# Kernel tuning notes

Hardware: AMD Instinct MI355X
Metric: run time of the kernel (lower is better)

Reference implementation:

```python
import jax, jax.numpy as jnp
import numpy as np

B, S, D, H = 1, 4096, 1024, 16
HD = D // H  # head_dim = 64


def setup_inputs() -> dict:
    key = jax.random.key(0)
    k1, k2, k3 = jax.random.split(key, 3)
    scale = 0.02
    return {
        "x": jax.random.normal(k1, (B, S, D), dtype=jnp.float32),
        "w_qkv": jax.random.normal(k2, (D, 3 * D), dtype=jnp.float32) * scale,
        "b_qkv": jnp.zeros((3 * D,), dtype=jnp.float32),
        "w_proj": jax.random.normal(k3, (D, D), dtype=jnp.float32) * scale,
        "b_proj": jnp.zeros((D,), dtype=jnp.float32),
    }


def reference(x, w_qkv, b_qkv, w_proj, b_proj):
    b, s, d = x.shape
    qkv = x @ w_qkv + b_qkv                      # [b, s, 3d]
    q, k, v = jnp.split(qkv, 3, axis=-1)
    # [b, h, s, hd]
    q = q.reshape(b, s, H, HD).transpose(0, 2, 1, 3)
    k = k.reshape(b, s, H, HD).transpose(0, 2, 1, 3)
    v = v.reshape(b, s, H, HD).transpose(0, 2, 1, 3)
    score = jnp.einsum("bhqd,bhkd->bhqk", q, k) / jnp.sqrt(jnp.float32(HD))
    causal = jnp.tril(jnp.ones((s, s), dtype=bool))
    score = jnp.where(causal, score, -jnp.inf)
    attn = jax.nn.softmax(score, axis=-1)        # dropout omitted (eval mode, p effectively 0)
    out = jnp.einsum("bhqk,bhkd->bhqd", attn, v)  # [b, h, s, hd]
    out = out.transpose(0, 2, 1, 3).reshape(b, s, d)
    return out @ w_proj + b_proj
```

## Files before the change

kernel.cpp:

```cpp
#include <hip/hip_runtime.h>
#include <hip/hip_bf16.h>
#include <math.h>

typedef __bf16 bf16;
typedef __bf16 bf16x8 __attribute__((ext_vector_type(8)));
typedef __bf16 bf16x4 __attribute__((ext_vector_type(4)));
typedef float f32x4 __attribute__((ext_vector_type(4)));

#define S_ 4096
#define D_ 1024
#define H_ 16
#define HD_ 64
#define N3_ 3072

typedef const __attribute__((address_space(1))) void* gas1_t;
typedef __attribute__((address_space(3))) void* las3_t;
static __device__ __forceinline__ void g2l16(const void* g, void* l) {
  __builtin_amdgcn_global_load_lds((gas1_t)g, (las3_t)l, 16, 0, 0);
}

__global__ __launch_bounds__(256) void cvt_f32_bf16(const float* __restrict__ in,
                                                    bf16* __restrict__ out) {
  int i = (blockIdx.x * 256 + threadIdx.x) * 4;
  float4 v = *(const float4*)(in + i);
  bf16x4 o;
  o.x = (bf16)v.x; o.y = (bf16)v.y; o.z = (bf16)v.z; o.w = (bf16)v.w;
  *(bf16x4*)(out + i) = o;
}

__global__ __launch_bounds__(256) void transpose_f32_bf16(const float* __restrict__ in,
                                                          bf16* __restrict__ out,
                                                          int R, int C, int ldin, int col0) {
  __shared__ float t[32][33];
  int bx = blockIdx.x * 32;
  int by = blockIdx.y * 32;
  int tx = threadIdx.x & 31, ty = threadIdx.x >> 5;
#pragma unroll
  for (int i = 0; i < 4; ++i)
    t[ty + i * 8][tx] = in[(size_t)(by + ty + i * 8) * ldin + col0 + bx + tx];
  __syncthreads();
#pragma unroll
  for (int i = 0; i < 4; ++i)
    out[(size_t)(bx + ty + i * 8) * R + by + tx] = (bf16)t[tx][ty + i * 8];
}

__global__ __launch_bounds__(256) void transpose_bf16(const bf16* __restrict__ in,
                                                      bf16* __restrict__ out,
                                                      int R, int C, int ldin, int col0) {
  __shared__ bf16 t[32][33];
  int bx = blockIdx.x * 32;
  int by = blockIdx.y * 32;
  int tx = threadIdx.x & 31, ty = threadIdx.x >> 5;
#pragma unroll
  for (int i = 0; i < 4; ++i)
    t[ty + i * 8][tx] = in[(size_t)(by + ty + i * 8) * ldin + col0 + bx + tx];
  __syncthreads();
#pragma unroll
  for (int i = 0; i < 4; ++i)
    out[(size_t)(bx + ty + i * 8) * R + by + tx] = t[tx][ty + i * 8];
}

__global__ __launch_bounds__(256) void gemm_bt(const bf16* __restrict__ A,
                                               const bf16* __restrict__ Bt,
                                               const float* __restrict__ bias,
                                               bf16* __restrict__ outb,
                                               float* __restrict__ outf,
                                               int M, int N, int K) {
  __shared__ bf16 sA[128 * 32];
  __shared__ bf16 sB[128 * 32];
  const int tid = threadIdx.x;
  const int wave = tid >> 6, lane = tid & 63;
  const int col = lane & 15, quad = lane >> 4;
  const int wm = (wave & 1) * 64, wn = (wave >> 1) * 64;
  const long bm = (long)blockIdx.x * 128, bn = (long)blockIdx.y * 128;
  const int srow = tid >> 2;
  const int soff = (tid & 3) * 8;

  f32x4 acc[4][4] = {};

  for (int kb = 0; kb < K; kb += 32) {
    __syncthreads();
    g2l16(A  + (bm + srow) * (long)K + kb + soff,      &sA[tid * 8]);
    g2l16(A  + (bm + 64 + srow) * (long)K + kb + soff, &sA[2048 + tid * 8]);
    g2l16(Bt + (bn + srow) * (long)K + kb + soff,      &sB[tid * 8]);
    g2l16(Bt + (bn + 64 + srow) * (long)K + kb + soff, &sB[2048 + tid * 8]);
    __syncthreads();

    bf16x8 af[4], bfr[4];
#pragma unroll
    for (int t = 0; t < 4; ++t) {
      af[t]  = *(const bf16x8*)(&sA[(wm + t * 16 + col) * 32 + quad * 8]);
      bfr[t] = *(const bf16x8*)(&sB[(wn + t * 16 + col) * 32 + quad * 8]);
    }
#pragma unroll
    for (int mt = 0; mt < 4; ++mt)
#pragma unroll
      for (int nt = 0; nt < 4; ++nt)
        acc[mt][nt] = __builtin_amdgcn_mfma_f32_16x16x32_bf16(af[mt], bfr[nt], acc[mt][nt], 0, 0, 0);
  }

#pragma unroll
  for (int mt = 0; mt < 4; ++mt) {
#pragma unroll
    for (int nt = 0; nt < 4; ++nt) {
      long gn = bn + wn + nt * 16 + col;
      float bv = bias ? bias[gn] : 0.f;
#pragma unroll
      for (int i = 0; i < 4; ++i) {
        long gm = bm + wm + mt * 16 + quad * 4 + i;
        float v = acc[mt][nt][i] + bv;
        if (outf) outf[gm * N + gn] = v;
        else      outb[gm * N + gn] = (bf16)v;
      }
    }
  }
}

__device__ __forceinline__ int swz_g(int row) {
  return (row & 3) | ((((row >> 2) ^ (row >> 3)) & 1) << 2);
}

__global__ __launch_bounds__(256) void attn_kernel(const bf16* __restrict__ qkv,
                                                   const bf16* __restrict__ vT,
                                                   bf16* __restrict__ Opart,
                                                   float* __restrict__ lws) {
  __shared__ bf16 sK[2][64 * 64];
  __shared__ bf16 sV[2][64 * 64];
  const int hh = blockIdx.x;
  const int qb = (int)(gridDim.y - 1 - blockIdx.y);
  const int sp = blockIdx.z;
  const int tid = threadIdx.x;
  const int wave = tid >> 6, lane = tid & 63;
  const int col = lane & 15, quad = lane >> 4;
  const int qbase = qb * 128 + wave * 32;

  const bf16* qp0 = qkv + (size_t)(qbase + col) * N3_ + hh * HD_;
  bf16x8 aq[2][2];
  aq[0][0] = *(const bf16x8*)(qp0 + quad * 8);
  aq[0][1] = *(const bf16x8*)(qp0 + 32 + quad * 8);
  aq[1][0] = *(const bf16x8*)(qp0 + 16 * N3_ + quad * 8);
  aq[1][1] = *(const bf16x8*)(qp0 + 16 * N3_ + 32 + quad * 8);

  f32x4 acc[2][4] = {};
  float l_part[2] = {0.f, 0.f};

  const bf16* kgbase = qkv + D_ + hh * HD_;
  const bf16* vgbase = vT + (size_t)hh * HD_ * S_;
  const int krow = (col >> 2) * 8 + (col & 3);
  const float CSCALE = 0.125f * 1.44269504088896f;
  const int it0 = sp ? (qb + 1) : 0;
  const int it1 = sp ? 2 * (qb + 1) : (qb + 1);

  const int srow = tid >> 2;
  const int sc0 = (tid & 3) * 2;
  const int gs = swz_g(srow);
  const int soff0 = srow * 64 + ((sc0 ^ gs) * 8);
  const int soff1 = srow * 64 + (((sc0 + 1) ^ gs) * 8);

  {
    const bf16* kg = kgbase + (size_t)(it0 * 64 + srow) * N3_ + sc0 * 8;
    const bf16* vg = vgbase + (size_t)srow * S_ + it0 * 64 + sc0 * 8;
    *(int4*)(&sK[0][soff0]) = *(const int4*)kg;
    *(int4*)(&sK[0][soff1]) = *(const int4*)(kg + 8);
    *(int4*)(&sV[0][soff0]) = *(const int4*)vg;
    *(int4*)(&sV[0][soff1]) = *(const int4*)(vg + 8);
  }
  __syncthreads();

  for (int j = it0; j < it1; ++j) {
    const int kb = j * 64;
    const int cur = (j - it0) & 1;
    const bool more = (j + 1 < it1);
    int4 pk0, pk1, pv0, pv1;
    if (more) {
      const bf16* kg = kgbase + (size_t)(kb + 64 + srow) * N3_ + sc0 * 8;
      const bf16* vg = vgbase + (size_t)srow * S_ + kb + 64 + sc0 * 8;
      pk0 = *(const int4*)kg; pk1 = *(const int4*)(kg + 8);
      pv0 = *(const int4*)vg; pv1 = *(const int4*)(vg + 8);
    }

    if (kb < qbase + 32) {
      const bool act0 = kb < qbase + 16;
      const bf16* kc = &sK[cur][0];
      const bf16* vc = &sV[cur][0];

      f32x4 st[2][4];
#pragma unroll
      for (int t = 0; t < 4; ++t) {
        int row = (t >> 1) * 32 + (t & 1) * 4 + krow;
        int pc = quad ^ swz_g(row);
        bf16x8 bk0 = *(const bf16x8*)(kc + row * 64 + pc * 8);
        bf16x8 bk1 = *(const bf16x8*)(kc + row * 64 + (pc ^ 4) * 8);
        if (act0) {
          f32x4 z = {};
          z = __builtin_amdgcn_mfma_f32_16x16x32_bf16(bk0, aq[0][0], z, 0, 0, 0);
          st[0][t] = __builtin_amdgcn_mfma_f32_16x16x32_bf16(bk1, aq[0][1], z, 0, 0, 0);
        }
        f32x4 z = {};
        z = __builtin_amdgcn_mfma_f32_16x16x32_bf16(bk0, aq[1][0], z, 0, 0, 0);
        st[1][t] = __builtin_amdgcn_mfma_f32_16x16x32_bf16(bk1, aq[1][1], z, 0, 0, 0);
      }

      bf16x8 pfrag[2][2];
#pragma unroll
      for (int s2 = 0; s2 < 2; ++s2) {
        if (s2 == 0 && !act0) continue;
        const int rowbase = qbase + 16 * s2;
        float p[4][4];
        if (kb + 63 <= rowbase) {
#pragma unroll
          for (int t = 0; t < 4; ++t)
#pragma unroll
            for (int r = 0; r < 4; ++r)
              p[t][r] = __builtin_amdgcn_exp2f(st[s2][t][r] * CSCALE);
        } else {
#pragma unroll
          for (int t = 0; t < 4; ++t)
#pragma unroll
            for (int r = 0; r < 4; ++r) {
              int key = kb + (t >> 1) * 32 + quad * 8 + (t & 1) * 4 + r;
              p[t][r] = (key > rowbase + col)
                            ? 0.f
                            : __builtin_amdgcn_exp2f(st[s2][t][r] * CSCALE);
            }
        }
#pragma unroll
        for (int t = 0; t < 4; ++t)
#pragma unroll
          for (int r = 0; r < 4; ++r) l_part[s2] += p[t][r];
#pragma unroll
        for (int c = 0; c < 2; ++c)
#pragma unroll
          for (int j2 = 0; j2 < 4; ++j2) {
            pfrag[s2][c][j2]     = (bf16)p[2 * c][j2];
            pfrag[s2][c][j2 + 4] = (bf16)p[2 * c + 1][j2];
          }
      }

#pragma unroll
      for (int c = 0; c < 2; ++c) {
#pragma unroll
        for (int n = 0; n < 4; ++n) {
          int row = n * 16 + col;
          int pc = (4 * c + quad) ^ swz_g(row);
          bf16x8 bv = *(const bf16x8*)(vc + row * 64 + pc * 8);
          if (act0)
            acc[0][n] = __builtin_amdgcn_mfma_f32_16x16x32_bf16(pfrag[0][c], bv, acc[0][n], 0, 0, 0);
          acc[1][n] = __builtin_amdgcn_mfma_f32_16x16x32_bf16(pfrag[1][c], bv, acc[1][n], 0, 0, 0);
        }
      }
    }

    if (more) {
      bf16* kn = &sK[cur ^ 1][0];
      bf16* vn = &sV[cur ^ 1][0];
      *(int4*)(kn + soff0) = pk0;
      *(int4*)(kn + soff1) = pk1;
      *(int4*)(vn + soff0) = pv0;
      *(int4*)(vn + soff1) = pv1;
    }
    __syncthreads();
  }

  bf16* Op = Opart + (size_t)sp * S_ * D_;
#pragma unroll
  for (int s2 = 0; s2 < 2; ++s2) {
    float l = l_part[s2];
    l += __shfl_xor(l, 16);
    l += __shfl_xor(l, 32);
    if (quad == 0)
      lws[((size_t)sp * H_ + hh) * S_ + qbase + 16 * s2 + col] = l;
#pragma unroll
    for (int n = 0; n < 4; ++n)
#pragma unroll
      for (int r = 0; r < 4; ++r)
        Op[(size_t)(qbase + 16 * s2 + quad * 4 + r) * D_ + hh * HD_ + n * 16 + col] =
            (bf16)acc[s2][n][r];
  }
}

__global__ __launch_bounds__(256) void attn_combine(const bf16* __restrict__ Opart,
                                                    const float* __restrict__ lws,
                                                    bf16* __restrict__ outb) {
  int e = (blockIdx.x * 256 + threadIdx.x) * 8;
  int s = e >> 10;
  int d = e & (D_ - 1);
  int h = d >> 6;
  float l = lws[(size_t)h * S_ + s] + lws[((size_t)H_ + h) * S_ + s];
  float inv = 1.0f / l;
  bf16x8 a = *(const bf16x8*)(Opart + e);
  bf16x8 b = *(const bf16x8*)(Opart + (size_t)S_ * D_ + e);
  bf16x8 o;
#pragma unroll
  for (int j = 0; j < 8; ++j)
    o[j] = (bf16)(((float)a[j] + (float)b[j]) * inv);
  *(bf16x8*)(outb + e) = o;
}

extern "C" void kernel_launch(void* const* d_in, const int* in_sizes, int n_in,
                              void* d_out, int out_size, void* d_ws, size_t ws_size,
                              hipStream_t stream) {
  const float* x      = (const float*)d_in[0];
  const float* w_qkv  = (const float*)d_in[1];
  const float* b_qkv  = (const float*)d_in[2];
  const float* w_proj = (const float*)d_in[3];
  const float* b_proj = (const float*)d_in[4];
  float* out = (float*)d_out;

  bf16* xb     = (bf16*)d_ws;
  bf16* wqkvT  = xb + (size_t)S_ * D_;
  bf16* wprojT = wqkvT + (size_t)N3_ * D_;
  bf16* qkv    = wprojT + (size_t)D_ * D_;
  bf16* vT     = qkv + (size_t)S_ * N3_;
  bf16* attn   = vT + (size_t)D_ * S_;
  bf16* Opart  = attn + (size_t)S_ * D_;
  float* lws   = (float*)(Opart + (size_t)2 * S_ * D_);

  cvt_f32_bf16<<<dim3((S_ * D_) / 1024), 256, 0, stream>>>(x, xb);
  transpose_f32_bf16<<<dim3(N3_ / 32, D_ / 32), 256, 0, stream>>>(w_qkv, wqkvT, D_, N3_, N3_, 0);
  transpose_f32_bf16<<<dim3(D_ / 32, D_ / 32), 256, 0, stream>>>(w_proj, wprojT, D_, D_, D_, 0);
  gemm_bt<<<dim3(S_ / 128, N3_ / 128), 256, 0, stream>>>(xb, wqkvT, b_qkv, qkv, nullptr,
                                                         S_, N3_, D_);
  transpose_bf16<<<dim3(D_ / 32, S_ / 32), 256, 0, stream>>>(qkv, vT, S_, D_, N3_, 2 * D_);
  attn_kernel<<<dim3(H_, S_ / 128, 2), 256, 0, stream>>>(qkv, vT, Opart, lws);
  attn_combine<<<dim3((S_ * D_) / 2048), 256, 0, stream>>>(Opart, lws, attn);
  gemm_bt<<<dim3(S_ / 128, D_ / 128), 256, 0, stream>>>(attn, wprojT, b_proj, nullptr, out,
                                                        S_, D_, D_);
}
```

Measured before the change: 223.2 us.

## Fold softmax scale into QKV GEMM, compute row sums via MFMA, narrow proj tile

The softmax scale (1/sqrt(hd)·log2e) is now applied to Q in the QKV GEMM epilogue, so the attention inner loop no longer multiplies every score before exp2. Per-row sums of P are computed with an extra MFMA against a ones vector instead of scalar adds plus cross-lane shuffles. The GEMM is templated on the N tile, and the output projection uses a 64-wide tile to launch more blocks. The trade-offs are extra MFMA work in the attention loop and Q being rounded to bf16 after scaling, which changes rounding slightly.

```diff
diff --git a/kernel.cpp b/kernel.cpp
--- a/kernel.cpp
+++ b/kernel.cpp
@@ -60,55 +60,61 @@
     out[(size_t)(bx + ty + i * 8) * R + by + tx] = t[tx][ty + i * 8];
 }
 
+template <int BN>
 __global__ __launch_bounds__(256) void gemm_bt(const bf16* __restrict__ A,
                                                const bf16* __restrict__ Bt,
                                                const float* __restrict__ bias,
                                                bf16* __restrict__ outb,
                                                float* __restrict__ outf,
-                                               int M, int N, int K) {
+                                               int M, int N, int K,
+                                               int qlim, float qscale) {
+  constexpr int NT = BN / 32;
   __shared__ bf16 sA[128 * 32];
-  __shared__ bf16 sB[128 * 32];
+  __shared__ bf16 sB[BN * 32];
   const int tid = threadIdx.x;
   const int wave = tid >> 6, lane = tid & 63;
   const int col = lane & 15, quad = lane >> 4;
-  const int wm = (wave & 1) * 64, wn = (wave >> 1) * 64;
-  const long bm = (long)blockIdx.x * 128, bn = (long)blockIdx.y * 128;
+  const int wm = (wave & 1) * 64, wn = (wave >> 1) * (BN / 2);
+  const long bm = (long)blockIdx.x * 128, bn = (long)blockIdx.y * BN;
   const int srow = tid >> 2;
   const int soff = (tid & 3) * 8;
 
-  f32x4 acc[4][4] = {};
+  f32x4 acc[4][NT] = {};
 
   for (int kb = 0; kb < K; kb += 32) {
     __syncthreads();
-    g2l16(A  + (bm + srow) * (long)K + kb + soff,      &sA[tid * 8]);
-    g2l16(A  + (bm + 64 + srow) * (long)K + kb + soff, &sA[2048 + tid * 8]);
-    g2l16(Bt + (bn + srow) * (long)K + kb + soff,      &sB[tid * 8]);
-    g2l16(Bt + (bn + 64 + srow) * (long)K + kb + soff, &sB[2048 + tid * 8]);
+    g2l16(A + (bm + srow) * (long)K + kb + soff,      &sA[tid * 8]);
+    g2l16(A + (bm + 64 + srow) * (long)K + kb + soff, &sA[2048 + tid * 8]);
+#pragma unroll
+    for (int i = 0; i < BN / 64; ++i)
+      g2l16(Bt + (bn + i * 64 + srow) * (long)K + kb + soff, &sB[i * 2048 + tid * 8]);
     __syncthreads();
 
-    bf16x8 af[4], bfr[4];
-#pragma unroll
-    for (int t = 0; t < 4; ++t) {
-      af[t]  = *(const bf16x8*)(&sA[(wm + t * 16 + col) * 32 + quad * 8]);
+    bf16x8 af[4], bfr[NT];
+#pragma unroll
+    for (int t = 0; t < 4; ++t)
+      af[t] = *(const bf16x8*)(&sA[(wm + t * 16 + col) * 32 + quad * 8]);
+#pragma unroll
+    for (int t = 0; t < NT; ++t)
       bfr[t] = *(const bf16x8*)(&sB[(wn + t * 16 + col) * 32 + quad * 8]);
-    }
 #pragma unroll
     for (int mt = 0; mt < 4; ++mt)
 #pragma unroll
-      for (int nt = 0; nt < 4; ++nt)
+      for (int nt = 0; nt < NT; ++nt)
         acc[mt][nt] = __builtin_amdgcn_mfma_f32_16x16x32_bf16(af[mt], bfr[nt], acc[mt][nt], 0, 0, 0);
   }
 
 #pragma unroll
   for (int mt = 0; mt < 4; ++mt) {
 #pragma unroll
-    for (int nt = 0; nt < 4; ++nt) {
+    for (int nt = 0; nt < NT; ++nt) {
       long gn = bn + wn + nt * 16 + col;
       float bv = bias ? bias[gn] : 0.f;
+      float sc = (gn < qlim) ? qscale : 1.0f;
 #pragma unroll
       for (int i = 0; i < 4; ++i) {
         long gm = bm + wm + mt * 16 + quad * 4 + i;
-        float v = acc[mt][nt][i] + bv;
+        float v = (acc[mt][nt][i] + bv) * sc;
         if (outf) outf[gm * N + gn] = v;
         else      outb[gm * N + gn] = (bf16)v;
       }
@@ -141,13 +147,16 @@
   aq[1][0] = *(const bf16x8*)(qp0 + 16 * N3_ + quad * 8);
   aq[1][1] = *(const bf16x8*)(qp0 + 16 * N3_ + 32 + quad * 8);
 
+  bf16x8 ones;
+#pragma unroll
+  for (int j = 0; j < 8; ++j) ones[j] = (bf16)1.0f;
+
   f32x4 acc[2][4] = {};
-  float l_part[2] = {0.f, 0.f};
+  f32x4 acc_l[2] = {};
 
   const bf16* kgbase = qkv + D_ + hh * HD_;
   const bf16* vgbase = vT + (size_t)hh * HD_ * S_;
   const int krow = (col >> 2) * 8 + (col & 3);
-  const float CSCALE = 0.125f * 1.44269504088896f;
   const int it0 = sp ? (qb + 1) : 0;
   const int it1 = sp ? 2 * (qb + 1) : (qb + 1);
 
@@ -212,7 +221,7 @@
           for (int t = 0; t < 4; ++t)
 #pragma unroll
             for (int r = 0; r < 4; ++r)
-              p[t][r] = __builtin_amdgcn_exp2f(st[s2][t][r] * CSCALE);
+              p[t][r] = __builtin_amdgcn_exp2f(st[s2][t][r]);
         } else {
 #pragma unroll
           for (int t = 0; t < 4; ++t)
@@ -221,13 +230,9 @@
               int key = kb + (t >> 1) * 32 + quad * 8 + (t & 1) * 4 + r;
               p[t][r] = (key > rowbase + col)
                             ? 0.f
-                            : __builtin_amdgcn_exp2f(st[s2][t][r] * CSCALE);
+                            : __builtin_amdgcn_exp2f(st[s2][t][r]);
             }
         }
-#pragma unroll
-        for (int t = 0; t < 4; ++t)
-#pragma unroll
-          for (int r = 0; r < 4; ++r) l_part[s2] += p[t][r];
 #pragma unroll
         for (int c = 0; c < 2; ++c)
 #pragma unroll
@@ -248,6 +253,9 @@
             acc[0][n] = __builtin_amdgcn_mfma_f32_16x16x32_bf16(pfrag[0][c], bv, acc[0][n], 0, 0, 0);
           acc[1][n] = __builtin_amdgcn_mfma_f32_16x16x32_bf16(pfrag[1][c], bv, acc[1][n], 0, 0, 0);
         }
+        if (act0)
+          acc_l[0] = __builtin_amdgcn_mfma_f32_16x16x32_bf16(pfrag[0][c], ones, acc_l[0], 0, 0, 0);
+        acc_l[1] = __builtin_amdgcn_mfma_f32_16x16x32_bf16(pfrag[1][c], ones, acc_l[1], 0, 0, 0);
       }
     }
 
@@ -265,16 +273,17 @@
   bf16* Op = Opart + (size_t)sp * S_ * D_;
 #pragma unroll
   for (int s2 = 0; s2 < 2; ++s2) {
-    float l = l_part[s2];
-    l += __shfl_xor(l, 16);
-    l += __shfl_xor(l, 32);
-    if (quad == 0)
-      lws[((size_t)sp * H_ + hh) * S_ + qbase + 16 * s2 + col] = l;
+    const int rowbase = qbase + 16 * s2;
+    if (col == 0) {
+#pragma unroll
+      for (int r = 0; r < 4; ++r)
+        lws[((size_t)sp * H_ + hh) * S_ + rowbase + quad * 4 + r] = acc_l[s2][r];
+    }
 #pragma unroll
     for (int n = 0; n < 4; ++n)
 #pragma unroll
       for (int r = 0; r < 4; ++r)
-        Op[(size_t)(qbase + 16 * s2 + quad * 4 + r) * D_ + hh * HD_ + n * 16 + col] =
+        Op[(size_t)(rowbase + quad * 4 + r) * D_ + hh * HD_ + n * 16 + col] =
             (bf16)acc[s2][n][r];
   }
 }
@@ -316,14 +325,16 @@
   bf16* Opart  = attn + (size_t)S_ * D_;
   float* lws   = (float*)(Opart + (size_t)2 * S_ * D_);
 
+  const float QSCALE = 0.125f * 1.44269504088896f;
+
   cvt_f32_bf16<<<dim3((S_ * D_) / 1024), 256, 0, stream>>>(x, xb);
   transpose_f32_bf16<<<dim3(N3_ / 32, D_ / 32), 256, 0, stream>>>(w_qkv, wqkvT, D_, N3_, N3_, 0);
   transpose_f32_bf16<<<dim3(D_ / 32, D_ / 32), 256, 0, stream>>>(w_proj, wprojT, D_, D_, D_, 0);
-  gemm_bt<<<dim3(S_ / 128, N3_ / 128), 256, 0, stream>>>(xb, wqkvT, b_qkv, qkv, nullptr,
-                                                         S_, N3_, D_);
+  gemm_bt<128><<<dim3(S_ / 128, N3_ / 128), 256, 0, stream>>>(
+      xb, wqkvT, b_qkv, qkv, nullptr, S_, N3_, D_, D_, QSCALE);
   transpose_bf16<<<dim3(D_ / 32, S_ / 32), 256, 0, stream>>>(qkv, vT, S_, D_, N3_, 2 * D_);
   attn_kernel<<<dim3(H_, S_ / 128, 2), 256, 0, stream>>>(qkv, vT, Opart, lws);
   attn_combine<<<dim3((S_ * D_) / 2048), 256, 0, stream>>>(Opart, lws, attn);
-  gemm_bt<<<dim3(S_ / 128, D_ / 128), 256, 0, stream>>>(attn, wprojT, b_proj, nullptr, out,
-                                                        S_, D_, D_);
-}
+  gemm_bt<64><<<dim3(S_ / 128, D_ / 64), 256, 0, stream>>>(
+      attn, wprojT, b_proj, nullptr, out, S_, D_, D_, 0, 1.0f);
+}
```

Result: faster. 214.9 us (-3.7%).
